# Optimization experiments

Measured on AMD Instinct MI355X. Metric: run time of the kernel, lower is better.

## Reference

```python
import jax, jax.numpy as jnp
import numpy as np

B, LC, LQ, D = 32, 2048, 256, 256


def setup_inputs() -> dict:
    key = jax.random.key(0)
    kc, kq, kcm, kqm, kw = jax.random.split(key, 5)
    context = jax.random.normal(kc, (B, LC, D), dtype=jnp.float32)
    query = jax.random.normal(kq, (B, LQ, D), dtype=jnp.float32)
    # True = masked (matches torch masked_fill semantics)
    context_mask = jax.random.randint(kcm, (B, LC), 0, 2).astype(bool)
    query_mask = jax.random.randint(kqm, (B, LQ), 0, 2).astype(bool)
    # nn.Linear(3*dim, 1, bias=False) weight, flattened to (3D,)
    w0 = jax.random.normal(kw, (3 * D,), dtype=jnp.float32) * (1.0 / np.sqrt(3 * D))
    return {"context": context, "query": query, "context_mask": context_mask,
            "query_mask": query_mask, "w0": w0}


def reference(context, query, context_mask, query_mask, w0):
    d = context.shape[-1]
    wc, wq, wm = w0[:d], w0[d:2 * d], w0[2 * d:]
    # trilinear sim: w0 . [c, q, c*q]  ==  c.wc + q.wq + (c*wm) q^T
    sc = context @ wc                                   # (B, Lc)
    sq = query @ wq                                     # (B, Lq)
    sim = sc[:, :, None] + sq[:, None, :] + jnp.einsum(
        'bcd,bqd->bcq', context * wm, query)            # (B, Lc, Lq)
    mask = context_mask[:, :, None] | query_mask[:, None, :]
    sim = jnp.where(mask, jnp.float32(-1e30), sim)
    S = jax.nn.softmax(sim, axis=-1)                    # row softmax over Lq
    SS = jax.nn.softmax(sim, axis=1)                    # col softmax over Lc
    S = jnp.nan_to_num(S)
    SS = jnp.nan_to_num(SS)
    A = jnp.einsum('bcq,bqd->bcd', S, query)            # (B, Lc, D)
    T = jnp.einsum('bkq,bkd->bqd', SS, context)         # SS^T @ context, (B, Lq, D)
    Bmat = jnp.einsum('bcq,bqd->bcd', S, T)             # (B, Lc, D)
    return (A, Bmat)
```

## Files before the change

kernel.cpp:

```cpp
#include <hip/hip_runtime.h>

#define B_  32
#define LC_ 2048
#define LQ_ 256
#define D_  256
#define NEGH (-30000.0f)

typedef _Float16 f16;
typedef _Float16 f16x4 __attribute__((ext_vector_type(4)));
typedef _Float16 f16x8 __attribute__((ext_vector_type(8)));
typedef float    f32x4 __attribute__((ext_vector_type(4)));

__global__ __launch_bounds__(256) void k_prep(
    const float* __restrict__ ctx, const float* __restrict__ qry,
    const float* __restrict__ w0, f16* __restrict__ ctx16,
    f16* __restrict__ qrywm16, float* __restrict__ sc, float* __restrict__ sq)
{
    const int lane = threadIdx.x & 63;
    const int wave = threadIdx.x >> 6;
    const int row  = blockIdx.x * 4 + wave;
    const int NC = B_ * LC_;
    if (row < NC) {
        float4 v = *(const float4*)(ctx + (long long)row * D_ + lane * 4);
        f16x4 h; h[0] = (f16)v.x; h[1] = (f16)v.y; h[2] = (f16)v.z; h[3] = (f16)v.w;
        *(f16x4*)(ctx16 + (long long)row * D_ + lane * 4) = h;
        float4 wc = *(const float4*)(w0 + lane * 4);
        float s = v.x*wc.x + v.y*wc.y + v.z*wc.z + v.w*wc.w;
        #pragma unroll
        for (int off = 32; off > 0; off >>= 1) s += __shfl_down(s, off, 64);
        if (lane == 0) sc[row] = s;
    } else {
        int r = row - NC;
        float4 v = *(const float4*)(qry + (long long)r * D_ + lane * 4);
        float4 wm = *(const float4*)(w0 + 2 * D_ + lane * 4);
        f16x4 h;
        h[0] = (f16)(v.x * wm.x); h[1] = (f16)(v.y * wm.y);
        h[2] = (f16)(v.z * wm.z); h[3] = (f16)(v.w * wm.w);
        *(f16x4*)(qrywm16 + (long long)r * D_ + lane * 4) = h;
        float4 wq = *(const float4*)(w0 + D_ + lane * 4);
        float s = v.x*wq.x + v.y*wq.y + v.z*wq.z + v.w*wq.w;
        #pragma unroll
        for (int off = 32; off > 0; off >>= 1) s += __shfl_down(s, off, 64);
        if (lane == 0) sq[r] = s;
    }
}

__global__ __launch_bounds__(256) void k_tq(
    const float* __restrict__ in, f16* __restrict__ out)
{
    __shared__ float tile[64 * 65];
    const int b = blockIdx.z;
    const int r0 = blockIdx.x * 64, c0 = blockIdx.y * 64;
    const int t = threadIdx.x;
    const float* ib = in + (long long)b * LQ_ * D_;
    #pragma unroll
    for (int p = 0; p < 4; ++p) {
        int r = (t >> 4) + p * 16;
        int cb = (t & 15) * 4;
        float4 v = *(const float4*)(ib + (long long)(r0 + r) * D_ + c0 + cb);
        tile[r * 65 + cb + 0] = v.x;
        tile[r * 65 + cb + 1] = v.y;
        tile[r * 65 + cb + 2] = v.z;
        tile[r * 65 + cb + 3] = v.w;
    }
    __syncthreads();
    f16* ob = out + (long long)b * 512 * LQ_;
    #pragma unroll
    for (int p = 0; p < 4; ++p) {
        int c = (t >> 4) + p * 16;
        int rb = (t & 15) * 4;
        f16x4 h;
        h[0] = (f16)tile[(rb + 0) * 65 + c];
        h[1] = (f16)tile[(rb + 1) * 65 + c];
        h[2] = (f16)tile[(rb + 2) * 65 + c];
        h[3] = (f16)tile[(rb + 3) * 65 + c];
        *(f16x4*)(ob + (long long)(c0 + c) * LQ_ + r0 + rb) = h;
    }
}

#define LDA1 40
__global__ __launch_bounds__(256) void k_g1(
    const f16* __restrict__ ctx16, const f16* __restrict__ qrywm16,
    const float* __restrict__ sc, const float* __restrict__ sq,
    const int* __restrict__ cmask, const int* __restrict__ qmask,
    f16* __restrict__ sim16,
    float* __restrict__ rowm, float* __restrict__ rowinvl,
    float* __restrict__ pm, float* __restrict__ pl)
{
    __shared__ f16 As[128 * LDA1];
    __shared__ f16 Bs[256 * LDA1];
    __shared__ float rowpm[4][64], rowps[4][64];
    __shared__ float colpm[4][128], colps[4][128];
    __shared__ float rowmax_s[128], colmax_s[256];
    const int b = blockIdx.z;
    const int c0 = blockIdx.x * 128;
    const int t = threadIdx.x, lane = t & 63, wv = t >> 6;
    const int wm_off = (wv >> 1) * 64, wn_off = (wv & 1) * 128;
    const f16* Ab = ctx16 + ((long long)b * LC_ + c0) * D_;
    const f16* Bb = qrywm16 + (long long)b * LQ_ * D_;
    const int srow = t >> 2, scg = (t & 3) * 8;
    f32x4 acc[4][8] = {};
    for (int k0 = 0; k0 < D_; k0 += 32) {
        #pragma unroll
        for (int p = 0; p < 2; ++p) {
            int r = srow + p * 64;
            *(f16x8*)(As + r * LDA1 + scg) = *(const f16x8*)(Ab + (long long)r * D_ + k0 + scg);
        }
        #pragma unroll
        for (int p = 0; p < 4; ++p) {
            int r = srow + p * 64;
            *(f16x8*)(Bs + r * LDA1 + scg) = *(const f16x8*)(Bb + (long long)r * D_ + k0 + scg);
        }
        __syncthreads();
        f16x8 af[4], bf[8];
        #pragma unroll
        for (int i = 0; i < 4; ++i)
            af[i] = *(const f16x8*)(As + (wm_off + i * 16 + (lane & 15)) * LDA1 + (lane >> 4) * 8);
        #pragma unroll
        for (int j = 0; j < 8; ++j)
            bf[j] = *(const f16x8*)(Bs + (wn_off + j * 16 + (lane & 15)) * LDA1 + (lane >> 4) * 8);
        #pragma unroll
        for (int i = 0; i < 4; ++i)
            #pragma unroll
            for (int j = 0; j < 8; ++j)
                acc[i][j] = __builtin_amdgcn_mfma_f32_16x16x32_f16(af[i], bf[j], acc[i][j], 0, 0, 0);
        __syncthreads();
    }
    float sqv[8]; int qmv[8];
    #pragma unroll
    for (int j = 0; j < 8; ++j) {
        int q = wn_off + j * 16 + (lane & 15);
        sqv[j] = sq[b * LQ_ + q];
        qmv[j] = qmask[b * LQ_ + q];
    }
    float scv_[4][4]; int cmv_[4][4];
    #pragma unroll
    for (int i = 0; i < 4; ++i)
        #pragma unroll
        for (int r = 0; r < 4; ++r) {
            int c = c0 + wm_off + i * 16 + (lane >> 4) * 4 + r;
            scv_[i][r] = sc[b * LC_ + c];
            cmv_[i][r] = cmask[b * LC_ + c];
        }
    float rmax[4][4], cmax[8];
    #pragma unroll
    for (int i = 0; i < 4; ++i)
        #pragma unroll
        for (int r = 0; r < 4; ++r) rmax[i][r] = -INFINITY;
    #pragma unroll
    for (int j = 0; j < 8; ++j) cmax[j] = -INFINITY;
    #pragma unroll
    for (int i = 0; i < 4; ++i) {
        #pragma unroll
        for (int r = 0; r < 4; ++r) {
            int c = c0 + wm_off + i * 16 + (lane >> 4) * 4 + r;
            f16* orow = sim16 + ((long long)b * LC_ + c) * LQ_ + wn_off + (lane & 15);
            #pragma unroll
            for (int j = 0; j < 8; ++j) {
                float val = (cmv_[i][r] | qmv[j]) ? NEGH : (acc[i][j][r] + scv_[i][r] + sqv[j]);
                f16 hh = (f16)val;
                orow[j * 16] = hh;
                float vr = (float)hh;
                rmax[i][r] = fmaxf(rmax[i][r], vr);
                cmax[j]    = fmaxf(cmax[j], vr);
            }
        }
    }
    #pragma unroll
    for (int i = 0; i < 4; ++i)
        #pragma unroll
        for (int r = 0; r < 4; ++r) {
            rmax[i][r] = fmaxf(rmax[i][r], __shfl_xor(rmax[i][r], 1, 64));
            rmax[i][r] = fmaxf(rmax[i][r], __shfl_xor(rmax[i][r], 2, 64));
            rmax[i][r] = fmaxf(rmax[i][r], __shfl_xor(rmax[i][r], 4, 64));
            rmax[i][r] = fmaxf(rmax[i][r], __shfl_xor(rmax[i][r], 8, 64));
        }
    #pragma unroll
    for (int j = 0; j < 8; ++j) {
        cmax[j] = fmaxf(cmax[j], __shfl_xor(cmax[j], 16, 64));
        cmax[j] = fmaxf(cmax[j], __shfl_xor(cmax[j], 32, 64));
    }
    if ((lane & 15) == 0) {
        #pragma unroll
        for (int i = 0; i < 4; ++i)
            #pragma unroll
            for (int r = 0; r < 4; ++r)
                rowpm[wv][i * 16 + (lane >> 4) * 4 + r] = rmax[i][r];
    }
    if (lane < 16) {
        #pragma unroll
        for (int j = 0; j < 8; ++j) colpm[wv][j * 16 + lane] = cmax[j];
    }
    __syncthreads();
    if (t < 128)
        rowmax_s[t] = fmaxf(rowpm[2 * (t >> 6)][t & 63], rowpm[2 * (t >> 6) + 1][t & 63]);
    colmax_s[t] = fmaxf(colpm[t >> 7][t & 127], colpm[(t >> 7) + 2][t & 127]);
    __syncthreads();
    float rmf[4][4], cmf[8];
    #pragma unroll
    for (int i = 0; i < 4; ++i)
        #pragma unroll
        for (int r = 0; r < 4; ++r)
            rmf[i][r] = rowmax_s[wm_off + i * 16 + (lane >> 4) * 4 + r];
    #pragma unroll
    for (int j = 0; j < 8; ++j) cmf[j] = colmax_s[wn_off + j * 16 + (lane & 15)];
    float rsum[4][4] = {}, csum[8] = {};
    #pragma unroll
    for (int i = 0; i < 4; ++i) {
        #pragma unroll
        for (int r = 0; r < 4; ++r) {
            #pragma unroll
            for (int j = 0; j < 8; ++j) {
                float val = (cmv_[i][r] | qmv[j]) ? NEGH : (acc[i][j][r] + scv_[i][r] + sqv[j]);
                float vr = (float)(f16)val;
                rsum[i][r] += __expf(vr - rmf[i][r]);
                csum[j]    += __expf(vr - cmf[j]);
            }
        }
    }
    #pragma unroll
    for (int i = 0; i < 4; ++i)
        #pragma unroll
        for (int r = 0; r < 4; ++r) {
            rsum[i][r] += __shfl_xor(rsum[i][r], 1, 64);
            rsum[i][r] += __shfl_xor(rsum[i][r], 2, 64);
            rsum[i][r] += __shfl_xor(rsum[i][r], 4, 64);
            rsum[i][r] += __shfl_xor(rsum[i][r], 8, 64);
        }
    #pragma unroll
    for (int j = 0; j < 8; ++j) {
        csum[j] += __shfl_xor(csum[j], 16, 64);
        csum[j] += __shfl_xor(csum[j], 32, 64);
    }
    if ((lane & 15) == 0) {
        #pragma unroll
        for (int i = 0; i < 4; ++i)
            #pragma unroll
            for (int r = 0; r < 4; ++r)
                rowps[wv][i * 16 + (lane >> 4) * 4 + r] = rsum[i][r];
    }
    if (lane < 16) {
        #pragma unroll
        for (int j = 0; j < 8; ++j) colps[wv][j * 16 + lane] = csum[j];
    }
    __syncthreads();
    if (t < 128) {
        float l = rowps[2 * (t >> 6)][t & 63] + rowps[2 * (t >> 6) + 1][t & 63];
        rowm[b * LC_ + c0 + t]    = rowmax_s[t];
        rowinvl[b * LC_ + c0 + t] = 1.0f / l;
    }
    {
        int idx = (b * 16 + blockIdx.x) * LQ_ + t;
        pm[idx] = colmax_s[t];
        pl[idx] = colps[t >> 7][t & 127] + colps[(t >> 7) + 2][t & 127];
    }
}

__global__ __launch_bounds__(256) void k_colreduce(
    const float* __restrict__ pm, const float* __restrict__ pl,
    float* __restrict__ colm, float* __restrict__ colinvl)
{
    const int col = blockIdx.x * 256 + threadIdx.x;
    const int b = col >> 8, q = col & 255;
    float M = -INFINITY, L = 0.f;
    for (int ch = 0; ch < 16; ++ch) {
        int idx = (b * 16 + ch) * LQ_ + q;
        float m = pm[idx], l = pl[idx];
        float nM = fmaxf(M, m);
        L = L * __expf(M - nM) + l * __expf(m - nM);
        M = nM;
    }
    colm[col] = M; colinvl[col] = 1.0f / L;
}

#define LDA3 66
#define G3SPLIT 4
#define G3CHUNK (LC_ / G3SPLIT)
__global__ __launch_bounds__(256) void k_g3(
    const f16* __restrict__ ctx16, const f16* __restrict__ sim16,
    const float* __restrict__ colm, float* __restrict__ Tpart)
{
    __shared__ f16 As[128 * LDA3];
    __shared__ f16 Bs[64 * LDA3];
    __shared__ float colm_s[64];
    const int b = blockIdx.x;
    const int combo = blockIdx.y;
    const int qt = combo & 3, dh = combo >> 2;
    const int q0 = qt * 64, d0 = dh * 128;
    const int cbeg = blockIdx.z * G3CHUNK;
    const int t = threadIdx.x, lane = t & 63, wv = t >> 6;
    const int wm_off = (wv >> 1) * 64, wn_off = (wv & 1) * 32;
    if (t < 64) colm_s[t] = colm[b * LQ_ + q0 + t];
    __syncthreads();
    const f16* Ab = ctx16 + (long long)b * LC_ * D_;
    const f16* Sb = sim16 + (long long)b * LC_ * LQ_;
    f32x4 acc[4][2] = {};
    const int acc_ = t >> 4, ad8 = (t & 15) * 8;
    const int bcc = t >> 3, bq8 = (t & 7) * 8;
    f16x8 ha[4], hb[2];
    #pragma unroll
    for (int p = 0; p < 4; ++p)
        ha[p] = *(const f16x8*)(Ab + (long long)(cbeg + acc_ + p * 16) * D_ + d0 + ad8);
    #pragma unroll
    for (int p = 0; p < 2; ++p)
        hb[p] = *(const f16x8*)(Sb + (long long)(cbeg + bcc + p * 32) * LQ_ + q0 + bq8);
    for (int c0 = cbeg; c0 < cbeg + G3CHUNK; c0 += 64) {
        #pragma unroll
        for (int p = 0; p < 4; ++p) {
            int cc = acc_ + p * 16;
            #pragma unroll
            for (int j = 0; j < 8; ++j)
                As[(ad8 + j) * LDA3 + cc] = ha[p][j];
        }
        #pragma unroll
        for (int p = 0; p < 2; ++p) {
            int cc = bcc + p * 32;
            #pragma unroll
            for (int j = 0; j < 8; ++j)
                Bs[(bq8 + j) * LDA3 + cc] = (f16)__expf((float)hb[p][j] - colm_s[bq8 + j]);
        }
        if (c0 + 64 < cbeg + G3CHUNK) {
            #pragma unroll
            for (int p = 0; p < 4; ++p)
                ha[p] = *(const f16x8*)(Ab + (long long)(c0 + 64 + acc_ + p * 16) * D_ + d0 + ad8);
            #pragma unroll
            for (int p = 0; p < 2; ++p)
                hb[p] = *(const f16x8*)(Sb + (long long)(c0 + 64 + bcc + p * 32) * LQ_ + q0 + bq8);
        }
        __syncthreads();
        #pragma unroll
        for (int kk = 0; kk < 64; kk += 32) {
            f16x8 af[4], bf[2];
            #pragma unroll
            for (int i = 0; i < 4; ++i)
                af[i] = *(const f16x8*)(As + (wm_off + i * 16 + (lane & 15)) * LDA3 + kk + (lane >> 4) * 8);
            #pragma unroll
            for (int j = 0; j < 2; ++j)
                bf[j] = *(const f16x8*)(Bs + (wn_off + j * 16 + (lane & 15)) * LDA3 + kk + (lane >> 4) * 8);
            #pragma unroll
            for (int i = 0; i < 4; ++i)
                #pragma unroll
                for (int j = 0; j < 2; ++j)
                    acc[i][j] = __builtin_amdgcn_mfma_f32_16x16x32_f16(af[i], bf[j], acc[i][j], 0, 0, 0);
        }
        __syncthreads();
    }
    float* Tb = Tpart + ((long long)blockIdx.z * B_ + b) * (LQ_ * D_);
    #pragma unroll
    for (int i = 0; i < 4; ++i) {
        #pragma unroll
        for (int r = 0; r < 4; ++r) {
            int d = d0 + wm_off + i * 16 + (lane >> 4) * 4 + r;
            float* orow = Tb + (long long)d * LQ_ + q0 + wn_off + (lane & 15);
            #pragma unroll
            for (int j = 0; j < 2; ++j)
                orow[j * 16] = acc[i][j][r];
        }
    }
}

__global__ __launch_bounds__(256) void k_bnorm(
    const float* __restrict__ Tpart, const float* __restrict__ colinvl,
    f16* __restrict__ Bcat)
{
    const long long i4 = ((long long)blockIdx.x * 256 + threadIdx.x) * 4;
    const int q = (int)(i4 & 255);
    const int d = (int)((i4 >> 8) & 255);
    const int b = (int)(i4 >> 16);
    float4 s = *(const float4*)(Tpart + i4);
    #pragma unroll
    for (int p = 1; p < G3SPLIT; ++p) {
        float4 v = *(const float4*)(Tpart + (long long)p * (B_ * LQ_ * D_) + i4);
        s.x += v.x; s.y += v.y; s.z += v.z; s.w += v.w;
    }
    float4 ci = *(const float4*)(colinvl + b * LQ_ + q);
    f16x4 h;
    h[0] = (f16)(s.x * ci.x); h[1] = (f16)(s.y * ci.y);
    h[2] = (f16)(s.z * ci.z); h[3] = (f16)(s.w * ci.w);
    *(f16x4*)(Bcat + (long long)b * 512 * LQ_ + (long long)(256 + d) * LQ_ + q) = h;
}

__global__ __launch_bounds__(256) void k_g23(
    const f16* __restrict__ sim16, const float* __restrict__ rowm,
    const float* __restrict__ rowinvl, const f16* __restrict__ Bcat,
    float* __restrict__ outA, float* __restrict__ outB)
{
    __shared__ f16 As[128 * LDA1];
    __shared__ f16 Bs[128 * LDA1];
    const int b = blockIdx.z;
    const int c0 = blockIdx.x * 128, n0 = blockIdx.y * 128;
    const int t = threadIdx.x, lane = t & 63, wv = t >> 6;
    const int wm_off = (wv >> 1) * 64, wn_off = (wv & 1) * 64;
    const f16* Ab = sim16 + ((long long)b * LC_ + c0) * LQ_;
    const f16* Bb = Bcat + ((long long)b * 512 + n0) * LQ_;
    const int srow = t >> 2, scg = (t & 3) * 8;
    float rm[2];
    #pragma unroll
    for (int p = 0; p < 2; ++p) rm[p] = rowm[b * LC_ + c0 + srow + p * 64];
    f32x4 acc[4][4] = {};
    f16x8 ha[2], hb[2];
    #pragma unroll
    for (int p = 0; p < 2; ++p) {
        int r = srow + p * 64;
        ha[p] = *(const f16x8*)(Ab + (long long)r * LQ_ + scg);
        hb[p] = *(const f16x8*)(Bb + (long long)r * LQ_ + scg);
    }
    for (int k0 = 0; k0 < LQ_; k0 += 32) {
        #pragma unroll
        for (int p = 0; p < 2; ++p) {
            int r = srow + p * 64;
            f16x8 e;
            #pragma unroll
            for (int j = 0; j < 8; ++j) e[j] = (f16)__expf((float)ha[p][j] - rm[p]);
            *(f16x8*)(As + r * LDA1 + scg) = e;
            *(f16x8*)(Bs + r * LDA1 + scg) = hb[p];
        }
        if (k0 + 32 < LQ_) {
            #pragma unroll
            for (int p = 0; p < 2; ++p) {
                int r = srow + p * 64;
                ha[p] = *(const f16x8*)(Ab + (long long)r * LQ_ + k0 + 32 + scg);
                hb[p] = *(const f16x8*)(Bb + (long long)r * LQ_ + k0 + 32 + scg);
            }
        }
        __syncthreads();
        f16x8 af[4], bf[4];
        #pragma unroll
        for (int i = 0; i < 4; ++i)
            af[i] = *(const f16x8*)(As + (wm_off + i * 16 + (lane & 15)) * LDA1 + (lane >> 4) * 8);
        #pragma unroll
        for (int j = 0; j < 4; ++j)
            bf[j] = *(const f16x8*)(Bs + (wn_off + j * 16 + (lane & 15)) * LDA1 + (lane >> 4) * 8);
        #pragma unroll
        for (int i = 0; i < 4; ++i)
            #pragma unroll
            for (int j = 0; j < 4; ++j)
                acc[i][j] = __builtin_amdgcn_mfma_f32_16x16x32_f16(af[i], bf[j], acc[i][j], 0, 0, 0);
        __syncthreads();
    }
    float* outp = (n0 < 256) ? outA : outB;
    const int nbase = (n0 < 256) ? n0 : (n0 - 256);
    #pragma unroll
    for (int i = 0; i < 4; ++i) {
        #pragma unroll
        for (int r = 0; r < 4; ++r) {
            int c = c0 + wm_off + i * 16 + (lane >> 4) * 4 + r;
            float ri = rowinvl[b * LC_ + c];
            float* orow = outp + ((long long)b * LC_ + c) * D_ + nbase + wn_off + (lane & 15);
            #pragma unroll
            for (int j = 0; j < 4; ++j)
                orow[j * 16] = acc[i][j][r] * ri;
        }
    }
}

extern "C" void kernel_launch(void* const* d_in, const int* in_sizes, int n_in,
                              void* d_out, int out_size, void* d_ws, size_t ws_size,
                              hipStream_t stream) {
    const float* ctx   = (const float*)d_in[0];
    const float* qry   = (const float*)d_in[1];
    const int*   cmask = (const int*)d_in[2];
    const int*   qmask = (const int*)d_in[3];
    const float* w0    = (const float*)d_in[4];
    float* out = (float*)d_out;

    char* w = (char*)d_ws;
    float* sc      = (float*)w;  w += (long long)65536 * 4;
    float* sq      = (float*)w;  w += (long long)8192 * 4;
    float* rowm    = (float*)w;  w += (long long)65536 * 4;
    float* rowinvl = (float*)w;  w += (long long)65536 * 4;
    float* colm    = (float*)w;  w += (long long)8192 * 4;
    float* colinvl = (float*)w;  w += (long long)8192 * 4;
    float* pm      = (float*)w;  w += (long long)524288 * 4;
    float* pl      = (float*)w;  w += (long long)524288 * 4;
    f16*   sim16   = (f16*)w;    w += (long long)16777216 * 2;
    f16*   ctx16   = (f16*)w;    w += (long long)16777216 * 2;
    f16*   qrywm16 = (f16*)w;    w += (long long)2097152 * 2;
    f16*   Bcat    = (f16*)w;    w += (long long)4194304 * 2;
    float* Tpart   = (float*)w;  w += (long long)G3SPLIT * 2097152 * 4;

    k_prep<<<18432, 256, 0, stream>>>(ctx, qry, w0, ctx16, qrywm16, sc, sq);
    k_tq<<<dim3(4, 4, 32), 256, 0, stream>>>(qry, Bcat);
    k_g1<<<dim3(16, 1, 32), 256, 0, stream>>>(ctx16, qrywm16, sc, sq, cmask, qmask,
        sim16, rowm, rowinvl, pm, pl);
    k_colreduce<<<32, 256, 0, stream>>>(pm, pl, colm, colinvl);
    k_g3<<<dim3(32, 8, G3SPLIT), 256, 0, stream>>>(ctx16, sim16, colm, Tpart);
    k_bnorm<<<2048, 256, 0, stream>>>(Tpart, colinvl, Bcat);
    k_g23<<<dim3(16, 4, 32), 256, 0, stream>>>(sim16, rowm, rowinvl, Bcat,
        out, out + (long long)B_ * LC_ * D_);
}
```

Baseline: 309.8 us.

## Precompute row-softmax numerators in g1, fold masks into biases, widen g1 to 512 threads

```diff
diff --git a/kernel.cpp b/kernel.cpp
--- a/kernel.cpp
+++ b/kernel.cpp
@@ -5,6 +5,7 @@
 #define LQ_ 256
 #define D_  256
 #define NEGH (-30000.0f)
+#define MASKF (-100000.0f)
 
 typedef _Float16 f16;
 typedef _Float16 f16x4 __attribute__((ext_vector_type(4)));
@@ -13,8 +14,10 @@
 
 __global__ __launch_bounds__(256) void k_prep(
     const float* __restrict__ ctx, const float* __restrict__ qry,
-    const float* __restrict__ w0, f16* __restrict__ ctx16,
-    f16* __restrict__ qrywm16, float* __restrict__ sc, float* __restrict__ sq)
+    const float* __restrict__ w0,
+    const int* __restrict__ cmask, const int* __restrict__ qmask,
+    f16* __restrict__ ctx16, f16* __restrict__ qrywm16,
+    float* __restrict__ scm, float* __restrict__ sqm)
 {
     const int lane = threadIdx.x & 63;
     const int wave = threadIdx.x >> 6;
@@ -28,7 +31,7 @@
         float s = v.x*wc.x + v.y*wc.y + v.z*wc.z + v.w*wc.w;
         #pragma unroll
         for (int off = 32; off > 0; off >>= 1) s += __shfl_down(s, off, 64);
-        if (lane == 0) sc[row] = s;
+        if (lane == 0) scm[row] = cmask[row] ? MASKF : s;
     } else {
         int r = row - NC;
         float4 v = *(const float4*)(qry + (long long)r * D_ + lane * 4);
@@ -41,7 +44,7 @@
         float s = v.x*wq.x + v.y*wq.y + v.z*wq.z + v.w*wq.w;
         #pragma unroll
         for (int off = 32; off > 0; off >>= 1) s += __shfl_down(s, off, 64);
-        if (lane == 0) sq[r] = s;
+        if (lane == 0) sqm[r] = qmask[r] ? MASKF : s;
     }
 }
 
@@ -79,76 +82,71 @@
 }
 
 #define LDA1 40
-__global__ __launch_bounds__(256) void k_g1(
+__global__ __launch_bounds__(512, 4) void k_g1(
     const f16* __restrict__ ctx16, const f16* __restrict__ qrywm16,
-    const float* __restrict__ sc, const float* __restrict__ sq,
-    const int* __restrict__ cmask, const int* __restrict__ qmask,
-    f16* __restrict__ sim16,
-    float* __restrict__ rowm, float* __restrict__ rowinvl,
+    const float* __restrict__ scm, const float* __restrict__ sqm,
+    f16* __restrict__ sim16, f16* __restrict__ p16,
+    float* __restrict__ rowinvl,
     float* __restrict__ pm, float* __restrict__ pl)
 {
     __shared__ f16 As[128 * LDA1];
     __shared__ f16 Bs[256 * LDA1];
-    __shared__ float rowpm[4][64], rowps[4][64];
-    __shared__ float colpm[4][128], colps[4][128];
+    __shared__ float rowpm[4][128], rowps[4][128];
+    __shared__ float colpm[2][256], colps[2][256];
     __shared__ float rowmax_s[128], colmax_s[256];
     const int b = blockIdx.z;
     const int c0 = blockIdx.x * 128;
     const int t = threadIdx.x, lane = t & 63, wv = t >> 6;
-    const int wm_off = (wv >> 1) * 64, wn_off = (wv & 1) * 128;
+    const int wm_off = (wv >> 2) * 64, wn_off = (wv & 3) * 64;
     const f16* Ab = ctx16 + ((long long)b * LC_ + c0) * D_;
     const f16* Bb = qrywm16 + (long long)b * LQ_ * D_;
     const int srow = t >> 2, scg = (t & 3) * 8;
-    f32x4 acc[4][8] = {};
+    f32x4 acc[4][4] = {};
+    f16x8 ha, hb0, hb1;
+    ha  = *(const f16x8*)(Ab + (long long)srow * D_ + scg);
+    hb0 = *(const f16x8*)(Bb + (long long)srow * D_ + scg);
+    hb1 = *(const f16x8*)(Bb + (long long)(srow + 128) * D_ + scg);
     for (int k0 = 0; k0 < D_; k0 += 32) {
-        #pragma unroll
-        for (int p = 0; p < 2; ++p) {
-            int r = srow + p * 64;
-            *(f16x8*)(As + r * LDA1 + scg) = *(const f16x8*)(Ab + (long long)r * D_ + k0 + scg);
-        }
-        #pragma unroll
-        for (int p = 0; p < 4; ++p) {
-            int r = srow + p * 64;
-            *(f16x8*)(Bs + r * LDA1 + scg) = *(const f16x8*)(Bb + (long long)r * D_ + k0 + scg);
-        }
-        __syncthreads();
-        f16x8 af[4], bf[8];
+        *(f16x8*)(As + srow * LDA1 + scg) = ha;
+        *(f16x8*)(Bs + srow * LDA1 + scg) = hb0;
+        *(f16x8*)(Bs + (srow + 128) * LDA1 + scg) = hb1;
+        if (k0 + 32 < D_) {
+            ha  = *(const f16x8*)(Ab + (long long)srow * D_ + k0 + 32 + scg);
+            hb0 = *(const f16x8*)(Bb + (long long)srow * D_ + k0 + 32 + scg);
+            hb1 = *(const f16x8*)(Bb + (long long)(srow + 128) * D_ + k0 + 32 + scg);
+        }
+        __syncthreads();
+        f16x8 af[4], bf[4];
         #pragma unroll
         for (int i = 0; i < 4; ++i)
             af[i] = *(const f16x8*)(As + (wm_off + i * 16 + (lane & 15)) * LDA1 + (lane >> 4) * 8);
         #pragma unroll
-        for (int j = 0; j < 8; ++j)
+        for (int j = 0; j < 4; ++j)
             bf[j] = *(const f16x8*)(Bs + (wn_off + j * 16 + (lane & 15)) * LDA1 + (lane >> 4) * 8);
         #pragma unroll
         for (int i = 0; i < 4; ++i)
             #pragma unroll
-            for (int j = 0; j < 8; ++j)
+            for (int j = 0; j < 4; ++j)
                 acc[i][j] = __builtin_amdgcn_mfma_f32_16x16x32_f16(af[i], bf[j], acc[i][j], 0, 0, 0);
         __syncthreads();
     }
-    float sqv[8]; int qmv[8];
-    #pragma unroll
-    for (int j = 0; j < 8; ++j) {
-        int q = wn_off + j * 16 + (lane & 15);
-        sqv[j] = sq[b * LQ_ + q];
-        qmv[j] = qmask[b * LQ_ + q];
-    }
-    float scv_[4][4]; int cmv_[4][4];
+    float sqv[4];
+    #pragma unroll
+    for (int j = 0; j < 4; ++j)
+        sqv[j] = sqm[b * LQ_ + wn_off + j * 16 + (lane & 15)];
+    float scv[4][4];
     #pragma unroll
     for (int i = 0; i < 4; ++i)
         #pragma unroll
-        for (int r = 0; r < 4; ++r) {
-            int c = c0 + wm_off + i * 16 + (lane >> 4) * 4 + r;
-            scv_[i][r] = sc[b * LC_ + c];
-            cmv_[i][r] = cmask[b * LC_ + c];
-        }
-    float rmax[4][4], cmax[8];
+        for (int r = 0; r < 4; ++r)
+            scv[i][r] = scm[b * LC_ + c0 + wm_off + i * 16 + (lane >> 4) * 4 + r];
+    float rmax[4][4], cmax[4];
     #pragma unroll
     for (int i = 0; i < 4; ++i)
         #pragma unroll
         for (int r = 0; r < 4; ++r) rmax[i][r] = -INFINITY;
     #pragma unroll
-    for (int j = 0; j < 8; ++j) cmax[j] = -INFINITY;
+    for (int j = 0; j < 4; ++j) cmax[j] = -INFINITY;
     #pragma unroll
     for (int i = 0; i < 4; ++i) {
         #pragma unroll
@@ -156,8 +154,8 @@
             int c = c0 + wm_off + i * 16 + (lane >> 4) * 4 + r;
             f16* orow = sim16 + ((long long)b * LC_ + c) * LQ_ + wn_off + (lane & 15);
             #pragma unroll
-            for (int j = 0; j < 8; ++j) {
-                float val = (cmv_[i][r] | qmv[j]) ? NEGH : (acc[i][j][r] + scv_[i][r] + sqv[j]);
+            for (int j = 0; j < 4; ++j) {
+                float val = fmaxf(acc[i][j][r] + scv[i][r] + sqv[j], NEGH);
                 f16 hh = (f16)val;
                 orow[j * 16] = hh;
                 float vr = (float)hh;
@@ -176,7 +174,7 @@
             rmax[i][r] = fmaxf(rmax[i][r], __shfl_xor(rmax[i][r], 8, 64));
         }
     #pragma unroll
-    for (int j = 0; j < 8; ++j) {
+    for (int j = 0; j < 4; ++j) {
         cmax[j] = fmaxf(cmax[j], __shfl_xor(cmax[j], 16, 64));
         cmax[j] = fmaxf(cmax[j], __shfl_xor(cmax[j], 32, 64));
     }
@@ -185,35 +183,40 @@
         for (int i = 0; i < 4; ++i)
             #pragma unroll
             for (int r = 0; r < 4; ++r)
-                rowpm[wv][i * 16 + (lane >> 4) * 4 + r] = rmax[i][r];
+                rowpm[wv & 3][wm_off + i * 16 + (lane >> 4) * 4 + r] = rmax[i][r];
     }
     if (lane < 16) {
         #pragma unroll
-        for (int j = 0; j < 8; ++j) colpm[wv][j * 16 + lane] = cmax[j];
+        for (int j = 0; j < 4; ++j) colpm[wv >> 2][wn_off + j * 16 + lane] = cmax[j];
     }
     __syncthreads();
     if (t < 128)
-        rowmax_s[t] = fmaxf(rowpm[2 * (t >> 6)][t & 63], rowpm[2 * (t >> 6) + 1][t & 63]);
-    colmax_s[t] = fmaxf(colpm[t >> 7][t & 127], colpm[(t >> 7) + 2][t & 127]);
+        rowmax_s[t] = fmaxf(fmaxf(rowpm[0][t], rowpm[1][t]), fmaxf(rowpm[2][t], rowpm[3][t]));
+    if (t < 256)
+        colmax_s[t] = fmaxf(colpm[0][t], colpm[1][t]);
     __syncthreads();
-    float rmf[4][4], cmf[8];
+    float rmf[4][4], cmf[4];
     #pragma unroll
     for (int i = 0; i < 4; ++i)
         #pragma unroll
         for (int r = 0; r < 4; ++r)
             rmf[i][r] = rowmax_s[wm_off + i * 16 + (lane >> 4) * 4 + r];
     #pragma unroll
-    for (int j = 0; j < 8; ++j) cmf[j] = colmax_s[wn_off + j * 16 + (lane & 15)];
-    float rsum[4][4] = {}, csum[8] = {};
+    for (int j = 0; j < 4; ++j) cmf[j] = colmax_s[wn_off + j * 16 + (lane & 15)];
+    float rsum[4][4] = {}, csum[4] = {};
     #pragma unroll
     for (int i = 0; i < 4; ++i) {
         #pragma unroll
         for (int r = 0; r < 4; ++r) {
-            #pragma unroll
-            for (int j = 0; j < 8; ++j) {
-                float val = (cmv_[i][r] | qmv[j]) ? NEGH : (acc[i][j][r] + scv_[i][r] + sqv[j]);
+            int c = c0 + wm_off + i * 16 + (lane >> 4) * 4 + r;
+            f16* prow = p16 + ((long long)b * LC_ + c) * LQ_ + wn_off + (lane & 15);
+            #pragma unroll
+            for (int j = 0; j < 4; ++j) {
+                float val = fmaxf(acc[i][j][r] + scv[i][r] + sqv[j], NEGH);
                 float vr = (float)(f16)val;
-                rsum[i][r] += __expf(vr - rmf[i][r]);
+                float er = __expf(vr - rmf[i][r]);
+                prow[j * 16] = (f16)er;
+                rsum[i][r] += er;
                 csum[j]    += __expf(vr - cmf[j]);
             }
         }
@@ -228,7 +231,7 @@
             rsum[i][r] += __shfl_xor(rsum[i][r], 8, 64);
         }
     #pragma unroll
-    for (int j = 0; j < 8; ++j) {
+    for (int j = 0; j < 4; ++j) {
         csum[j] += __shfl_xor(csum[j], 16, 64);
         csum[j] += __shfl_xor(csum[j], 32, 64);
     }
@@ -237,22 +240,21 @@
         for (int i = 0; i < 4; ++i)
             #pragma unroll
             for (int r = 0; r < 4; ++r)
-                rowps[wv][i * 16 + (lane >> 4) * 4 + r] = rsum[i][r];
+                rowps[wv & 3][wm_off + i * 16 + (lane >> 4) * 4 + r] = rsum[i][r];
     }
     if (lane < 16) {
         #pragma unroll
-        for (int j = 0; j < 8; ++j) colps[wv][j * 16 + lane] = csum[j];
+        for (int j = 0; j < 4; ++j) colps[wv >> 2][wn_off + j * 16 + lane] = csum[j];
     }
     __syncthreads();
     if (t < 128) {
-        float l = rowps[2 * (t >> 6)][t & 63] + rowps[2 * (t >> 6) + 1][t & 63];
-        rowm[b * LC_ + c0 + t]    = rowmax_s[t];
+        float l = rowps[0][t] + rowps[1][t] + rowps[2][t] + rowps[3][t];
         rowinvl[b * LC_ + c0 + t] = 1.0f / l;
     }
-    {
+    if (t < 256) {
         int idx = (b * 16 + blockIdx.x) * LQ_ + t;
         pm[idx] = colmax_s[t];
-        pl[idx] = colps[t >> 7][t & 127] + colps[(t >> 7) + 2][t & 127];
+        pl[idx] = colps[0][t] + colps[1][t];
     }
 }
 
@@ -380,9 +382,9 @@
     *(f16x4*)(Bcat + (long long)b * 512 * LQ_ + (long long)(256 + d) * LQ_ + q) = h;
 }
 
-__global__ __launch_bounds__(256) void k_g23(
-    const f16* __restrict__ sim16, const float* __restrict__ rowm,
-    const float* __restrict__ rowinvl, const f16* __restrict__ Bcat,
+__global__ __launch_bounds__(256, 4) void k_g23(
+    const f16* __restrict__ p16, const float* __restrict__ rowinvl,
+    const f16* __restrict__ Bcat,
     float* __restrict__ outA, float* __restrict__ outB)
 {
     __shared__ f16 As[128 * LDA1];
@@ -391,12 +393,9 @@
     const int c0 = blockIdx.x * 128, n0 = blockIdx.y * 128;
     const int t = threadIdx.x, lane = t & 63, wv = t >> 6;
     const int wm_off = (wv >> 1) * 64, wn_off = (wv & 1) * 64;
-    const f16* Ab = sim16 + ((long long)b * LC_ + c0) * LQ_;
+    const f16* Ab = p16 + ((long long)b * LC_ + c0) * LQ_;
     const f16* Bb = Bcat + ((long long)b * 512 + n0) * LQ_;
     const int srow = t >> 2, scg = (t & 3) * 8;
-    float rm[2];
-    #pragma unroll
-    for (int p = 0; p < 2; ++p) rm[p] = rowm[b * LC_ + c0 + srow + p * 64];
     f32x4 acc[4][4] = {};
     f16x8 ha[2], hb[2];
     #pragma unroll
@@ -409,10 +408,7 @@
         #pragma unroll
         for (int p = 0; p < 2; ++p) {
             int r = srow + p * 64;
-            f16x8 e;
-            #pragma unroll
-            for (int j = 0; j < 8; ++j) e[j] = (f16)__expf((float)ha[p][j] - rm[p]);
-            *(f16x8*)(As + r * LDA1 + scg) = e;
+            *(f16x8*)(As + r * LDA1 + scg) = ha[p];
             *(f16x8*)(Bs + r * LDA1 + scg) = hb[p];
         }
         if (k0 + 32 < LQ_) {
@@ -465,27 +461,27 @@
     float* out = (float*)d_out;
 
     char* w = (char*)d_ws;
-    float* sc      = (float*)w;  w += (long long)65536 * 4;
-    float* sq      = (float*)w;  w += (long long)8192 * 4;
-    float* rowm    = (float*)w;  w += (long long)65536 * 4;
+    float* scm     = (float*)w;  w += (long long)65536 * 4;
+    float* sqm     = (float*)w;  w += (long long)8192 * 4;
     float* rowinvl = (float*)w;  w += (long long)65536 * 4;
     float* colm    = (float*)w;  w += (long long)8192 * 4;
     float* colinvl = (float*)w;  w += (long long)8192 * 4;
     float* pm      = (float*)w;  w += (long long)524288 * 4;
     float* pl      = (float*)w;  w += (long long)524288 * 4;
     f16*   sim16   = (f16*)w;    w += (long long)16777216 * 2;
+    f16*   p16     = (f16*)w;    w += (long long)16777216 * 2;
     f16*   ctx16   = (f16*)w;    w += (long long)16777216 * 2;
     f16*   qrywm16 = (f16*)w;    w += (long long)2097152 * 2;
     f16*   Bcat    = (f16*)w;    w += (long long)4194304 * 2;
     float* Tpart   = (float*)w;  w += (long long)G3SPLIT * 2097152 * 4;
 
-    k_prep<<<18432, 256, 0, stream>>>(ctx, qry, w0, ctx16, qrywm16, sc, sq);
+    k_prep<<<18432, 256, 0, stream>>>(ctx, qry, w0, cmask, qmask, ctx16, qrywm16, scm, sqm);
     k_tq<<<dim3(4, 4, 32), 256, 0, stream>>>(qry, Bcat);
-    k_g1<<<dim3(16, 1, 32), 256, 0, stream>>>(ctx16, qrywm16, sc, sq, cmask, qmask,
-        sim16, rowm, rowinvl, pm, pl);
+    k_g1<<<dim3(16, 1, 32), 512, 0, stream>>>(ctx16, qrywm16, scm, sqm,
+        sim16, p16, rowinvl, pm, pl);
     k_colreduce<<<32, 256, 0, stream>>>(pm, pl, colm, colinvl);
     k_g3<<<dim3(32, 8, G3SPLIT), 256, 0, stream>>>(ctx16, sim16, colm, Tpart);
     k_bnorm<<<2048, 256, 0, stream>>>(Tpart, colinvl, Bcat);
-    k_g23<<<dim3(16, 4, 32), 256, 0, stream>>>(sim16, rowm, rowinvl, Bcat,
+    k_g23<<<dim3(16, 4, 32), 256, 0, stream>>>(p16, rowinvl, Bcat,
         out, out + (long long)B_ * LC_ * D_);
 }
```

New measurement: 312.7 us. No clear change (+0.9%).
